# Kernel tuning notes

Measured on AMD Instinct MI355X. Metric: run time of the kernel, lower is better.

## Reference

```python
import jax, jax.numpy as jnp
import numpy as np

FEATURE_DIM = 4
LOSS_WEIGHT = 1.0
DELTA_V = 0.5
DELTA_D = 1.5
NUM_LABELS = 8  # instance ids 0..7; 0 = background
B, H, W = 16, 640, 640


def _safe_norm(x, axis):
    # L2 norm with grad-safe sqrt (forward value exact: 0 when sum of squares is 0)
    sq = jnp.sum(x * x, axis=axis)
    pos = sq > 0
    return jnp.where(pos, jnp.sqrt(jnp.where(pos, sq, 1.0)), 0.0)


def _single_loss(emb, instance, kernel, training_mask):
    # emb: [H,W,C], instance: [H,W] int, kernel/training_mask: [H,W] float
    C = emb.shape[-1]
    L = NUM_LABELS
    tm = training_mask > 0.5
    kr = kernel > 0.5
    inst = jnp.where(tm, instance, 0).reshape(-1)          # [P]
    inst_k = jnp.where(kr.reshape(-1), inst, 0)            # [P]
    emb_f = emb.reshape(-1, C)                              # [P,C]

    # per-label kernel-region means (emb_mean), label 0 column is zeros
    sums = jax.ops.segment_sum(emb_f, inst_k, num_segments=L)                       # [L,C]
    cnts = jax.ops.segment_sum(jnp.ones(inst_k.shape, jnp.float32), inst_k, L)      # [L]
    mu = sums / jnp.maximum(cnts, 1.0)[:, None]
    mu = mu.at[0].set(0.0)

    # aggregation term: per-pixel distance to its instance mean
    d = _safe_norm(emb_f - mu[inst], axis=1)                                         # [P]
    term = jnp.log(jnp.maximum(d - DELTA_V, 0.0) ** 2 + 1.0)
    cnt_i = jax.ops.segment_sum(jnp.ones(inst.shape, jnp.float32), inst, L)
    agg = jax.ops.segment_sum(term, inst, L) / jnp.maximum(cnt_i, 1.0)               # [L]
    # original skips label 0, then takes mean of l_agg[1:] -> drops first nonzero label
    l_agg = jnp.mean(agg[2:])

    # discrimination term: all ordered pairs of distinct nonzero labels
    dd = _safe_norm(mu[:, None, :] - mu[None, :, :], axis=-1)                        # [L,L]
    valid = (1.0 - jnp.eye(L, dtype=jnp.float32)).at[0, :].set(0.0).at[:, 0].set(0.0)
    dis = jnp.log(jnp.maximum(2.0 * DELTA_D - dd, 0.0) ** 2 + 1.0)
    l_dis = jnp.sum(dis * valid) / jnp.sum(valid)

    l_reg = jnp.mean(jnp.log(_safe_norm(mu, axis=1) + 1.0)) * 0.001
    return l_agg + l_dis + l_reg


def reference(emb, instance, kernel, training_mask):
    losses = jax.vmap(_single_loss)(emb, instance, kernel, training_mask)  # [B]
    return LOSS_WEIGHT * jnp.mean(losses)


def setup_inputs() -> dict:
    key = jax.random.key(0)
    k1, k2, k3 = jax.random.split(key, 3)
    emb = jax.random.normal(k1, (B, H, W, FEATURE_DIM), dtype=jnp.float32)
    instance = jax.random.randint(k2, (B, H, W), 0, NUM_LABELS, dtype=jnp.int32)
    kernel = jax.random.uniform(k3, (B, H, W), dtype=jnp.float32)
    training_mask = jnp.ones((B, H, W), dtype=jnp.float32)
    return {"emb": emb, "instance": instance, "kernel": kernel, "training_mask": training_mask}
```

## Files before the change

### kernel.cpp

```cpp
#include <hip/hip_runtime.h>
#include <math.h>

#define NLAB 8
#define BATCH 16
#define S_OFF  0
#define CK_OFF 28
#define CI_OFF 35
#define AG_OFF 41
#define ACC_PER_B 48
#define ACC_FLOATS (BATCH * ACC_PER_B)
#define LAB_OFFSET 4096
#define GX 128
#define TSPAN (GX * 256)
#define ILP 4

typedef __attribute__((ext_vector_type(2))) float v2f;
typedef unsigned long long ull;

__device__ __forceinline__ v2f v2fma(v2f a, v2f b, v2f c) {
#if defined(__has_builtin) && __has_builtin(__builtin_elementwise_fma)
  return __builtin_elementwise_fma(a, b, c);
#else
  v2f r; r.x = fmaf(a.x, b.x, c.x); r.y = fmaf(a.y, b.y, c.y); return r;
#endif
}

__device__ __forceinline__ float wave_reduce(float v) {
#pragma unroll
  for (int off = 32; off > 0; off >>= 1) v += __shfl_xor(v, off, 64);
  return v;
}
__device__ __forceinline__ ull wr64(ull v) {
#pragma unroll
  for (int off = 32; off > 0; off >>= 1) v += __shfl_xor(v, off, 64);
  return v;
}

__global__ __launch_bounds__(256) void k_accum(
    const float4* __restrict__ emb, const int* __restrict__ inst,
    const float* __restrict__ ker, const float* __restrict__ tmk,
    float* __restrict__ acc, unsigned char* __restrict__ labc,
    int P, int use_cache)
{
  const int b = blockIdx.y;
  const size_t base = (size_t)b * P;
  const float4* e  = emb + base;
  const int*    ip = inst + base;
  const float*  kp = ker + base;
  const float*  tp = tmk + base;
  unsigned char* lb = labc + base;

  v2f s2[7][2];
#pragma unroll
  for (int j = 0; j < 7; ++j) { s2[j][0] = (v2f)(0.f); s2[j][1] = (v2f)(0.f); }
  ull ck64 = 0, ci64 = 0;

  const int tid = blockIdx.x * blockDim.x + threadIdx.x;

  int p0 = tid;
  for (; p0 + (ILP - 1) * TSPAN < P; p0 += ILP * TSPAN) {
    int   iv[ILP]; float tv[ILP], kv[ILP]; float4 ev[ILP];
#pragma unroll
    for (int k = 0; k < ILP; ++k) iv[k] = ip[p0 + k * TSPAN];
#pragma unroll
    for (int k = 0; k < ILP; ++k) tv[k] = tp[p0 + k * TSPAN];
#pragma unroll
    for (int k = 0; k < ILP; ++k) kv[k] = kp[p0 + k * TSPAN];
#pragma unroll
    for (int k = 0; k < ILP; ++k) ev[k] = e[p0 + k * TSPAN];

#pragma unroll
    for (int k = 0; k < ILP; ++k) {
      int lab = (tv[k] > 0.5f) ? (iv[k] & 7) : 0;
      int ki  = (kv[k] > 0.5f) ? 1 : 0;
      float kf = (float)ki;
      if (use_cache) lb[p0 + k * TSPAN] = (unsigned char)lab;
      ci64 += 1ull << (8 * lab);
      ck64 += (ull)ki << (8 * lab);
#pragma unroll
      for (int l = 1; l < NLAB; ++l) {
        float mk = (lab == l) ? kf : 0.f;
        v2f mk2; mk2.x = mk; mk2.y = mk;
        v2f e01; e01.x = ev[k].x; e01.y = ev[k].y;
        v2f e23; e23.x = ev[k].z; e23.y = ev[k].w;
        s2[l - 1][0] = v2fma(mk2, e01, s2[l - 1][0]);
        s2[l - 1][1] = v2fma(mk2, e23, s2[l - 1][1]);
      }
    }
  }
  for (int p = p0; p < P; p += TSPAN) {
    int   iv = ip[p];
    float tv = tp[p];
    float kv = kp[p];
    float4 ev = e[p];
    int lab = (tv > 0.5f) ? (iv & 7) : 0;
    int ki  = (kv > 0.5f) ? 1 : 0;
    float kf = (float)ki;
    if (use_cache) lb[p] = (unsigned char)lab;
    ci64 += 1ull << (8 * lab);
    ck64 += (ull)ki << (8 * lab);
#pragma unroll
    for (int l = 1; l < NLAB; ++l) {
      float mk = (lab == l) ? kf : 0.f;
      v2f mk2; mk2.x = mk; mk2.y = mk;
      v2f e01; e01.x = ev.x; e01.y = ev.y;
      v2f e23; e23.x = ev.z; e23.y = ev.w;
      s2[l - 1][0] = v2fma(mk2, e01, s2[l - 1][0]);
      s2[l - 1][1] = v2fma(mk2, e23, s2[l - 1][1]);
    }
  }

  __shared__ float red[4][48];
  const int wid = threadIdx.x >> 6, lane = threadIdx.x & 63;
#pragma unroll
  for (int j = 0; j < 7; ++j) {
    float v0 = wave_reduce(s2[j][0].x);
    float v1 = wave_reduce(s2[j][0].y);
    float v2 = wave_reduce(s2[j][1].x);
    float v3 = wave_reduce(s2[j][1].y);
    if (lane == 0) {
      red[wid][S_OFF + j * 4 + 0] = v0;
      red[wid][S_OFF + j * 4 + 1] = v1;
      red[wid][S_OFF + j * 4 + 2] = v2;
      red[wid][S_OFF + j * 4 + 3] = v3;
    }
  }
  {
    const ull M8 = 0x00FF00FF00FF00FFull;
    ull ckA = wr64(ck64 & M8);
    ull ckB = wr64((ck64 >> 8) & M8);
    ull ciA = wr64(ci64 & M8);
    ull ciB = wr64((ci64 >> 8) & M8);
    if (lane == 0) {
#pragma unroll
      for (int l = 1; l < NLAB; ++l) {
        ull v = (l & 1) ? (ckB >> (16 * (l >> 1))) : (ckA >> (16 * (l >> 1)));
        red[wid][CK_OFF + l - 1] = (float)(v & 0xFFFF);
      }
#pragma unroll
      for (int l = 2; l < NLAB; ++l) {
        ull v = (l & 1) ? (ciB >> (16 * (l >> 1))) : (ciA >> (16 * (l >> 1)));
        red[wid][CI_OFF + l - 2] = (float)(v & 0xFFFF);
      }
    }
  }
  __syncthreads();
  if (threadIdx.x < AG_OFF) {
    float v = red[0][threadIdx.x] + red[1][threadIdx.x] +
              red[2][threadIdx.x] + red[3][threadIdx.x];
    atomicAdd(acc + b * ACC_PER_B + threadIdx.x, v);
  }
}

__global__ __launch_bounds__(256) void k_agg(
    const float4* __restrict__ emb, const int* __restrict__ inst,
    const float* __restrict__ tmk, const unsigned char* __restrict__ labc,
    float* __restrict__ acc, int P, int use_cache)
{
  const int b = blockIdx.y;
  const size_t base = (size_t)b * P;
  __shared__ float4 smu[NLAB];
  const float* accB = acc + b * ACC_PER_B;
  if (threadIdx.x < NLAB) {
    int l = threadIdx.x;
    float4 m;
    if (l == 0) {
      m = make_float4(0.f, 0.f, 0.f, 0.f);
    } else {
      float inv = 1.f / fmaxf(accB[CK_OFF + l - 1], 1.f);
      m = make_float4(accB[S_OFF + (l - 1) * 4 + 0] * inv,
                      accB[S_OFF + (l - 1) * 4 + 1] * inv,
                      accB[S_OFF + (l - 1) * 4 + 2] * inv,
                      accB[S_OFF + (l - 1) * 4 + 3] * inv);
    }
    smu[l] = m;
  }
  __syncthreads();

  const float4* e = emb + base;
  const unsigned char* lb = labc + base;
  const int*   ip = inst + base;
  const float* tp = tmk + base;

  float aggl[6];
#pragma unroll
  for (int l = 0; l < 6; ++l) aggl[l] = 0.f;

  const int tid = blockIdx.x * blockDim.x + threadIdx.x;

  int p0 = tid;
  for (; p0 + (ILP - 1) * TSPAN < P; p0 += ILP * TSPAN) {
    int lab[ILP]; float4 ev[ILP];
    if (use_cache) {
#pragma unroll
      for (int k = 0; k < ILP; ++k) lab[k] = lb[p0 + k * TSPAN];
    } else {
      int iv[ILP]; float tv[ILP];
#pragma unroll
      for (int k = 0; k < ILP; ++k) iv[k] = ip[p0 + k * TSPAN];
#pragma unroll
      for (int k = 0; k < ILP; ++k) tv[k] = tp[p0 + k * TSPAN];
#pragma unroll
      for (int k = 0; k < ILP; ++k) lab[k] = (tv[k] > 0.5f) ? (iv[k] & 7) : 0;
    }
#pragma unroll
    for (int k = 0; k < ILP; ++k) ev[k] = e[p0 + k * TSPAN];

#pragma unroll
    for (int k = 0; k < ILP; ++k) {
      float4 mv = smu[lab[k]];
      float dx = ev[k].x - mv.x, dy = ev[k].y - mv.y;
      float dz = ev[k].z - mv.z, dw = ev[k].w - mv.w;
      float sq = dx * dx + dy * dy + dz * dz + dw * dw;
      float d  = sqrtf(sq);
      float t  = fmaxf(d - 0.5f, 0.f);
      float term = (lab[k] >= 2) ? logf(fmaf(t, t, 1.f)) : 0.f;
#pragma unroll
      for (int l = 0; l < 6; ++l) aggl[l] += (lab[k] == l + 2) ? term : 0.f;
    }
  }
  for (int p = p0; p < P; p += TSPAN) {
    int lab;
    if (use_cache) lab = lb[p];
    else           lab = (tp[p] > 0.5f) ? (ip[p] & 7) : 0;
    float4 ev = e[p];
    float4 mv = smu[lab];
    float dx = ev.x - mv.x, dy = ev.y - mv.y;
    float dz = ev.z - mv.z, dw = ev.w - mv.w;
    float d = sqrtf(dx * dx + dy * dy + dz * dz + dw * dw);
    float t = fmaxf(d - 0.5f, 0.f);
    float term = (lab >= 2) ? logf(fmaf(t, t, 1.f)) : 0.f;
#pragma unroll
    for (int l = 0; l < 6; ++l) aggl[l] += (lab == l + 2) ? term : 0.f;
  }

  __shared__ float red[4][8];
  const int wid = threadIdx.x >> 6, lane = threadIdx.x & 63;
#pragma unroll
  for (int l = 0; l < 6; ++l) {
    float v = wave_reduce(aggl[l]);
    if (lane == 0) red[wid][l] = v;
  }
  __syncthreads();
  if (threadIdx.x < 6) {
    float v = red[0][threadIdx.x] + red[1][threadIdx.x] +
              red[2][threadIdx.x] + red[3][threadIdx.x];
    atomicAdd(acc + b * ACC_PER_B + AG_OFF + threadIdx.x, v);
  }
}

__global__ void k_final(const float* __restrict__ acc, float* __restrict__ out, int nb) {
  const int lane = threadIdx.x;
  float loss = 0.f;
  if (lane < nb) {
    const float* a = acc + lane * ACC_PER_B;
    float mu[NLAB][4];
#pragma unroll
    for (int c = 0; c < 4; ++c) mu[0][c] = 0.f;
#pragma unroll
    for (int l = 1; l < NLAB; ++l) {
      float inv = 1.f / fmaxf(a[CK_OFF + l - 1], 1.f);
#pragma unroll
      for (int c = 0; c < 4; ++c) mu[l][c] = a[S_OFF + (l - 1) * 4 + c] * inv;
    }
    float l_agg = 0.f;
#pragma unroll
    for (int l = 2; l < NLAB; ++l)
      l_agg += a[AG_OFF + l - 2] / fmaxf(a[CI_OFF + l - 2], 1.f);
    l_agg *= (1.f / 6.f);
    float ssum = 0.f;
    for (int i = 1; i < NLAB; ++i)
      for (int j = 1; j < NLAB; ++j) {
        if (i == j) continue;
        float dx = mu[i][0] - mu[j][0], dy = mu[i][1] - mu[j][1];
        float dz = mu[i][2] - mu[j][2], dw = mu[i][3] - mu[j][3];
        float dd = sqrtf(dx * dx + dy * dy + dz * dz + dw * dw);
        float t = fmaxf(3.0f - dd, 0.f);
        ssum += logf(fmaf(t, t, 1.f));
      }
    float l_dis = ssum / 42.f;
    float rsum = 0.f;
#pragma unroll
    for (int l = 1; l < NLAB; ++l) {
      float n = sqrtf(mu[l][0] * mu[l][0] + mu[l][1] * mu[l][1] +
                      mu[l][2] * mu[l][2] + mu[l][3] * mu[l][3]);
      rsum += logf(n + 1.f);
    }
    float l_reg = rsum * (0.001f / NLAB);
    loss = l_agg + l_dis + l_reg;
  }
  loss = wave_reduce(loss);
  if (lane == 0) out[0] = loss / (float)nb;
}

extern "C" void kernel_launch(void* const* d_in, const int* in_sizes, int n_in,
                              void* d_out, int out_size, void* d_ws, size_t ws_size,
                              hipStream_t stream) {
  const float4* emb = (const float4*)d_in[0];
  const int*    inst = (const int*)d_in[1];
  const float*  ker  = (const float*)d_in[2];
  const float*  tmk  = (const float*)d_in[3];
  float* out = (float*)d_out;

  const int total = in_sizes[1];
  const int P = total / BATCH;

  float* acc = (float*)d_ws;
  unsigned char* labc = (unsigned char*)((char*)d_ws + LAB_OFFSET);
  const size_t need = (size_t)LAB_OFFSET + (size_t)total;
  const int use_cache = (ws_size >= need) ? 1 : 0;

  hipMemsetAsync(d_ws, 0, ACC_FLOATS * sizeof(float), stream);

  k_accum<<<dim3(GX, BATCH), 256, 0, stream>>>(emb, inst, ker, tmk, acc, labc, P, use_cache);
  k_agg  <<<dim3(GX, BATCH), 256, 0, stream>>>(emb, inst, tmk, labc, acc, P, use_cache);
  k_final<<<1, 64, 0, stream>>>(acc, out, BATCH);
}
```

Before: 243.8 us.

## Fuse accumulate, aggregate and final passes into one cooperative kernel with grid sync

Result: no change. 244.9 us (+0.5%).

```diff
diff --git a/kernel.cpp b/kernel.cpp
--- a/kernel.cpp
+++ b/kernel.cpp
@@ -1,5 +1,8 @@
 #include <hip/hip_runtime.h>
+#include <hip/hip_cooperative_groups.h>
 #include <math.h>
+
+namespace cg = cooperative_groups;
 
 #define NLAB 8
 #define BATCH 16
@@ -34,6 +37,245 @@
 #pragma unroll
   for (int off = 32; off > 0; off >>= 1) v += __shfl_xor(v, off, 64);
   return v;
+}
+
+__global__ __launch_bounds__(256) void k_fused(
+    const float4* __restrict__ emb, const int* __restrict__ inst,
+    const float* __restrict__ ker, const float* __restrict__ tmk,
+    float* __restrict__ acc, float* __restrict__ out, int P)
+{
+  cg::grid_group grid = cg::this_grid();
+  const int b = blockIdx.y;
+  const size_t base = (size_t)b * P;
+  const float4* e  = emb + base;
+  const int*    ip = inst + base;
+  const float*  kp = ker + base;
+  const float*  tp = tmk + base;
+
+  __shared__ float  red[4][48];
+  __shared__ float4 smu[NLAB];
+
+  const int tid = blockIdx.x * blockDim.x + threadIdx.x;
+  const int wid = threadIdx.x >> 6, lane = threadIdx.x & 63;
+
+  v2f s2[7][2];
+#pragma unroll
+  for (int j = 0; j < 7; ++j) { s2[j][0] = (v2f)(0.f); s2[j][1] = (v2f)(0.f); }
+  ull ck64 = 0, ci64 = 0;
+  ull packs = 0;
+
+  int jj = 0;
+  int p0 = tid;
+  for (; p0 + (ILP - 1) * TSPAN < P; p0 += ILP * TSPAN) {
+    int   iv[ILP]; float tv[ILP], kv[ILP]; float4 ev[ILP];
+#pragma unroll
+    for (int k = 0; k < ILP; ++k) iv[k] = ip[p0 + k * TSPAN];
+#pragma unroll
+    for (int k = 0; k < ILP; ++k) tv[k] = tp[p0 + k * TSPAN];
+#pragma unroll
+    for (int k = 0; k < ILP; ++k) kv[k] = kp[p0 + k * TSPAN];
+#pragma unroll
+    for (int k = 0; k < ILP; ++k) ev[k] = e[p0 + k * TSPAN];
+
+#pragma unroll
+    for (int k = 0; k < ILP; ++k) {
+      int lab = (tv[k] > 0.5f) ? (iv[k] & 7) : 0;
+      int ki  = (kv[k] > 0.5f) ? 1 : 0;
+      float kf = (float)ki;
+      packs |= (ull)lab << (4 * (jj + k));
+      ci64  += 1ull << (8 * lab);
+      ck64  += (ull)ki << (8 * lab);
+#pragma unroll
+      for (int l = 1; l < NLAB; ++l) {
+        float mk = (lab == l) ? kf : 0.f;
+        v2f mk2; mk2.x = mk; mk2.y = mk;
+        v2f e01; e01.x = ev[k].x; e01.y = ev[k].y;
+        v2f e23; e23.x = ev[k].z; e23.y = ev[k].w;
+        s2[l - 1][0] = v2fma(mk2, e01, s2[l - 1][0]);
+        s2[l - 1][1] = v2fma(mk2, e23, s2[l - 1][1]);
+      }
+    }
+    jj += ILP;
+  }
+  for (int p = p0; p < P; p += TSPAN) {
+    int   iv = ip[p];
+    float tv = tp[p];
+    float kv = kp[p];
+    float4 ev = e[p];
+    int lab = (tv > 0.5f) ? (iv & 7) : 0;
+    int ki  = (kv > 0.5f) ? 1 : 0;
+    float kf = (float)ki;
+    packs |= (ull)lab << (4 * jj);
+    ++jj;
+    ci64 += 1ull << (8 * lab);
+    ck64 += (ull)ki << (8 * lab);
+#pragma unroll
+    for (int l = 1; l < NLAB; ++l) {
+      float mk = (lab == l) ? kf : 0.f;
+      v2f mk2; mk2.x = mk; mk2.y = mk;
+      v2f e01; e01.x = ev.x; e01.y = ev.y;
+      v2f e23; e23.x = ev.z; e23.y = ev.w;
+      s2[l - 1][0] = v2fma(mk2, e01, s2[l - 1][0]);
+      s2[l - 1][1] = v2fma(mk2, e23, s2[l - 1][1]);
+    }
+  }
+
+#pragma unroll
+  for (int j = 0; j < 7; ++j) {
+    float v0 = wave_reduce(s2[j][0].x);
+    float v1 = wave_reduce(s2[j][0].y);
+    float v2 = wave_reduce(s2[j][1].x);
+    float v3 = wave_reduce(s2[j][1].y);
+    if (lane == 0) {
+      red[wid][S_OFF + j * 4 + 0] = v0;
+      red[wid][S_OFF + j * 4 + 1] = v1;
+      red[wid][S_OFF + j * 4 + 2] = v2;
+      red[wid][S_OFF + j * 4 + 3] = v3;
+    }
+  }
+  {
+    const ull M8 = 0x00FF00FF00FF00FFull;
+    ull ckA = wr64(ck64 & M8);
+    ull ckB = wr64((ck64 >> 8) & M8);
+    ull ciA = wr64(ci64 & M8);
+    ull ciB = wr64((ci64 >> 8) & M8);
+    if (lane == 0) {
+#pragma unroll
+      for (int l = 1; l < NLAB; ++l) {
+        ull v = (l & 1) ? (ckB >> (16 * (l >> 1))) : (ckA >> (16 * (l >> 1)));
+        red[wid][CK_OFF + l - 1] = (float)(v & 0xFFFF);
+      }
+#pragma unroll
+      for (int l = 2; l < NLAB; ++l) {
+        ull v = (l & 1) ? (ciB >> (16 * (l >> 1))) : (ciA >> (16 * (l >> 1)));
+        red[wid][CI_OFF + l - 2] = (float)(v & 0xFFFF);
+      }
+    }
+  }
+  __syncthreads();
+  if (threadIdx.x < AG_OFF) {
+    float v = red[0][threadIdx.x] + red[1][threadIdx.x] +
+              red[2][threadIdx.x] + red[3][threadIdx.x];
+    atomicAdd(acc + b * ACC_PER_B + threadIdx.x, v);
+  }
+
+  grid.sync();
+
+  {
+    const float* accB = acc + b * ACC_PER_B;
+    if (threadIdx.x < NLAB) {
+      int l = threadIdx.x;
+      float4 m;
+      if (l == 0) {
+        m = make_float4(0.f, 0.f, 0.f, 0.f);
+      } else {
+        float inv = 1.f / fmaxf(accB[CK_OFF + l - 1], 1.f);
+        m = make_float4(accB[S_OFF + (l - 1) * 4 + 0] * inv,
+                        accB[S_OFF + (l - 1) * 4 + 1] * inv,
+                        accB[S_OFF + (l - 1) * 4 + 2] * inv,
+                        accB[S_OFF + (l - 1) * 4 + 3] * inv);
+      }
+      smu[l] = m;
+    }
+  }
+  __syncthreads();
+
+  float aggl[6];
+#pragma unroll
+  for (int l = 0; l < 6; ++l) aggl[l] = 0.f;
+
+  jj = 0;
+  p0 = tid;
+  for (; p0 + (ILP - 1) * TSPAN < P; p0 += ILP * TSPAN) {
+    float4 ev[ILP];
+#pragma unroll
+    for (int k = 0; k < ILP; ++k) ev[k] = e[p0 + k * TSPAN];
+#pragma unroll
+    for (int k = 0; k < ILP; ++k) {
+      int lab = (int)((packs >> (4 * (jj + k))) & 7);
+      float4 mv = smu[lab];
+      float dx = ev[k].x - mv.x, dy = ev[k].y - mv.y;
+      float dz = ev[k].z - mv.z, dw = ev[k].w - mv.w;
+      float sq = dx * dx + dy * dy + dz * dz + dw * dw;
+      float d  = sqrtf(sq);
+      float t  = fmaxf(d - 0.5f, 0.f);
+      float term = (lab >= 2) ? logf(fmaf(t, t, 1.f)) : 0.f;
+#pragma unroll
+      for (int l = 0; l < 6; ++l) aggl[l] += (lab == l + 2) ? term : 0.f;
+    }
+    jj += ILP;
+  }
+  for (int p = p0; p < P; p += TSPAN) {
+    int lab = (int)((packs >> (4 * jj)) & 7);
+    ++jj;
+    float4 ev = e[p];
+    float4 mv = smu[lab];
+    float dx = ev.x - mv.x, dy = ev.y - mv.y;
+    float dz = ev.z - mv.z, dw = ev.w - mv.w;
+    float d = sqrtf(dx * dx + dy * dy + dz * dz + dw * dw);
+    float t = fmaxf(d - 0.5f, 0.f);
+    float term = (lab >= 2) ? logf(fmaf(t, t, 1.f)) : 0.f;
+#pragma unroll
+    for (int l = 0; l < 6; ++l) aggl[l] += (lab == l + 2) ? term : 0.f;
+  }
+
+  __syncthreads();
+#pragma unroll
+  for (int l = 0; l < 6; ++l) {
+    float v = wave_reduce(aggl[l]);
+    if (lane == 0) red[wid][l] = v;
+  }
+  __syncthreads();
+  if (threadIdx.x < 6) {
+    float v = red[0][threadIdx.x] + red[1][threadIdx.x] +
+              red[2][threadIdx.x] + red[3][threadIdx.x];
+    atomicAdd(acc + b * ACC_PER_B + AG_OFF + threadIdx.x, v);
+  }
+
+  grid.sync();
+
+  if (blockIdx.x == 0 && blockIdx.y == 0 && threadIdx.x < 64) {
+    float loss = 0.f;
+    if (lane < BATCH) {
+      const float* a = acc + lane * ACC_PER_B;
+      float mu[NLAB][4];
+#pragma unroll
+      for (int c = 0; c < 4; ++c) mu[0][c] = 0.f;
+#pragma unroll
+      for (int l = 1; l < NLAB; ++l) {
+        float inv = 1.f / fmaxf(a[CK_OFF + l - 1], 1.f);
+#pragma unroll
+        for (int c = 0; c < 4; ++c) mu[l][c] = a[S_OFF + (l - 1) * 4 + c] * inv;
+      }
+      float l_agg = 0.f;
+#pragma unroll
+      for (int l = 2; l < NLAB; ++l)
+        l_agg += a[AG_OFF + l - 2] / fmaxf(a[CI_OFF + l - 2], 1.f);
+      l_agg *= (1.f / 6.f);
+      float ssum = 0.f;
+      for (int i = 1; i < NLAB; ++i)
+        for (int j = 1; j < NLAB; ++j) {
+          if (i == j) continue;
+          float dx = mu[i][0] - mu[j][0], dy = mu[i][1] - mu[j][1];
+          float dz = mu[i][2] - mu[j][2], dw = mu[i][3] - mu[j][3];
+          float dd = sqrtf(dx * dx + dy * dy + dz * dz + dw * dw);
+          float t = fmaxf(3.0f - dd, 0.f);
+          ssum += logf(fmaf(t, t, 1.f));
+        }
+      float l_dis = ssum / 42.f;
+      float rsum = 0.f;
+#pragma unroll
+      for (int l = 1; l < NLAB; ++l) {
+        float n = sqrtf(mu[l][0] * mu[l][0] + mu[l][1] * mu[l][1] +
+                        mu[l][2] * mu[l][2] + mu[l][3] * mu[l][3]);
+        rsum += logf(n + 1.f);
+      }
+      float l_reg = rsum * (0.001f / NLAB);
+      loss = l_agg + l_dis + l_reg;
+    }
+    loss = wave_reduce(loss);
+    if (lane == 0) out[0] = loss / (float)BATCH;
+  }
 }
 
 __global__ __launch_bounds__(256) void k_accum(
@@ -303,16 +545,33 @@
   float* out = (float*)d_out;
 
   const int total = in_sizes[1];
-  const int P = total / BATCH;
+  int P = total / BATCH;
 
   float* acc = (float*)d_ws;
-  unsigned char* labc = (unsigned char*)((char*)d_ws + LAB_OFFSET);
-  const size_t need = (size_t)LAB_OFFSET + (size_t)total;
-  const int use_cache = (ws_size >= need) ? 1 : 0;
 
   hipMemsetAsync(d_ws, 0, ACC_FLOATS * sizeof(float), stream);
 
-  k_accum<<<dim3(GX, BATCH), 256, 0, stream>>>(emb, inst, ker, tmk, acc, labc, P, use_cache);
-  k_agg  <<<dim3(GX, BATCH), 256, 0, stream>>>(emb, inst, tmk, labc, acc, P, use_cache);
-  k_final<<<1, 64, 0, stream>>>(acc, out, BATCH);
-}
+  static int coop_bpc = -1;
+  if (coop_bpc < 0) {
+    int nb = 0;
+    if (hipOccupancyMaxActiveBlocksPerMultiprocessor(&nb, k_fused, 256, 0)
+        != hipSuccess) nb = 0;
+    coop_bpc = nb;
+  }
+
+  hipError_t cerr = hipErrorUnknown;
+  if (P <= 16 * TSPAN && coop_bpc >= 8) {
+    void* args[] = {(void*)&emb, (void*)&inst, (void*)&ker, (void*)&tmk,
+                    (void*)&acc, (void*)&out, (void*)&P};
+    cerr = hipLaunchCooperativeKernel((void*)k_fused, dim3(GX, BATCH),
+                                      dim3(256), args, 0, stream);
+  }
+  if (cerr != hipSuccess) {
+    unsigned char* labc = (unsigned char*)((char*)d_ws + LAB_OFFSET);
+    const size_t need = (size_t)LAB_OFFSET + (size_t)total;
+    const int use_cache = (ws_size >= need) ? 1 : 0;
+    k_accum<<<dim3(GX, BATCH), 256, 0, stream>>>(emb, inst, ker, tmk, acc, labc, P, use_cache);
+    k_agg  <<<dim3(GX, BATCH), 256, 0, stream>>>(emb, inst, tmk, labc, acc, P, use_cache);
+    k_final<<<1, 64, 0, stream>>>(acc, out, BATCH);
+  }
+}
```
